# Kernel optimization log

Measured on AMD Instinct MI355X. Metric: run time of the kernel, lower is better.

Reference implementation:

```python
import jax, jax.numpy as jnp
import numpy as np

B, S, D, H = 4, 2048, 1024, 16
DK = D // H

def setup_inputs() -> dict:
    key = jax.random.key(0)
    ks = jax.random.split(key, 11)
    s = 1.0 / np.sqrt(D)
    return {
        "query": jax.random.normal(ks[0], (B, S, D), jnp.float32),
        "key_": jax.random.normal(ks[1], (B, S, D), jnp.float32),
        "value": jax.random.normal(ks[2], (B, S, D), jnp.float32),
        "Wq": jax.random.uniform(ks[3], (D, D), jnp.float32, -s, s),
        "bq": jax.random.uniform(ks[4], (D,), jnp.float32, -s, s),
        "Wk": jax.random.uniform(ks[5], (D, D), jnp.float32, -s, s),
        "bk": jax.random.uniform(ks[6], (D,), jnp.float32, -s, s),
        "Wv": jax.random.uniform(ks[7], (D, D), jnp.float32, -s, s),
        "bv": jax.random.uniform(ks[8], (D,), jnp.float32, -s, s),
        "Wo": jax.random.uniform(ks[9], (D, D), jnp.float32, -s, s),
        "bo": jax.random.uniform(ks[10], (D,), jnp.float32, -s, s),
    }

def _split_heads(x):
    # [B,S,D] -> [B,H,S,DK]
    b, s, _ = x.shape
    return x.reshape(b, s, H, DK).transpose(0, 2, 1, 3)

def reference(query, key_, value, Wq, bq, Wk, bk, Wv, bv, Wo, bo):
    Q = _split_heads(query @ Wq.T + bq)
    K = _split_heads(key_ @ Wk.T + bk)
    V = _split_heads(value @ Wv.T + bv)
    scores = jnp.einsum('bhqd,bhkd->bhqk', Q, K) / np.sqrt(DK).astype(np.float32)
    attn = jax.nn.softmax(scores, axis=-1)
    ctx = jnp.einsum('bhqk,bhkd->bhqd', attn, V)  # [B,H,S,DK]
    ctx = ctx.transpose(0, 2, 1, 3).reshape(query.shape[0], -1, D)
    return ctx @ Wo.T + bo
```

## Files before the change

kernel.cpp:

```cpp
#include <hip/hip_runtime.h>
#include <hip/hip_bf16.h>
#include <math.h>


#define B_SZ   4
#define S_LEN  2048
#define D_DIM  1024
#define NH     16
#define DKD    64
#define M_TOT  (B_SZ * S_LEN)

typedef __bf16 bf16_t;
typedef bf16_t bf16x8 __attribute__((ext_vector_type(8)));
typedef bf16_t bf16x4 __attribute__((ext_vector_type(4)));
typedef float  f32x4  __attribute__((ext_vector_type(4)));

typedef __attribute__((address_space(1))) void gvoid;
typedef __attribute__((address_space(3))) void lvoid;

extern "C" __device__ float __ocml_native_exp2_f32(float);

__global__ __launch_bounds__(256)
void cvt_kernel(const float* __restrict__ src, bf16_t* __restrict__ dst, int n4)
{
    const int i = blockIdx.x * blockDim.x + threadIdx.x;
    if (i < n4) {
        f32x4 v = *(const f32x4*)(src + (size_t)i * 4);
        bf16x4 o;
        #pragma unroll
        for (int j = 0; j < 4; ++j) o[j] = (bf16_t)v[j];
        *(bf16x4*)(dst + (size_t)i * 4) = o;
    }
}

__global__ __launch_bounds__(256, 2)
void qkv_gemm(const float* __restrict__ Aq, const float* __restrict__ Ak,
              const float* __restrict__ Av,
              const bf16_t* __restrict__ Wqb, const bf16_t* __restrict__ Wkb,
              const bf16_t* __restrict__ Wvb,
              const float* __restrict__ bq, const float* __restrict__ bk,
              const float* __restrict__ bv,
              bf16_t* __restrict__ Qw, bf16_t* __restrict__ Kw,
              bf16_t* __restrict__ Vt, float qscale)
{
    constexpr int K = 1024, N = 1024;
    constexpr int BM = 128, BN = 128, BK = 32;

    __shared__ __align__(16) bf16_t lA[BM * BK];
    __shared__ __align__(16) bf16_t lB[BN * BK];

    const int z = blockIdx.z;
    const float* A  = (z == 0) ? Aq : (z == 1) ? Ak : Av;
    const bf16_t* W = (z == 0) ? Wqb : (z == 1) ? Wkb : Wvb;
    const float* bias = (z == 0) ? bq : (z == 1) ? bk : bv;
    const float scale = (z == 0) ? qscale : 1.0f;

    const int tid  = threadIdx.x;
    const int wave = tid >> 6;
    const int lane = tid & 63;

    const int row0 = blockIdx.x * BM;
    const int col0 = blockIdx.y * BN;

    const int wr = (wave >> 1) * 64;
    const int wc = (wave & 1) * 64;

    f32x4 acc[4][4] = {};

    const int frow = lane & 15;
    const int kq   = (lane >> 4) * 8;

    const int r0c = tid >> 2;
    const int k0c = (tid & 3) * 8;
    const int r1c = (256 + tid) >> 2;
    const int k1c = k0c;

    f32x4 pa[2][2];
    {
        const float* g0 = A + (size_t)(row0 + r0c) * K + k0c;
        const float* g1 = A + (size_t)(row0 + r1c) * K + k1c;
        pa[0][0] = *(const f32x4*)g0;  pa[0][1] = *(const f32x4*)(g0 + 4);
        pa[1][0] = *(const f32x4*)g1;  pa[1][1] = *(const f32x4*)(g1 + 4);
    }

    for (int k0 = 0; k0 < K; k0 += BK) {
        __syncthreads();
        #pragma unroll
        for (int p = 0; p < 2; ++p) {
            bf16x8 a8;
            #pragma unroll
            for (int j = 0; j < 4; ++j) {
                a8[j]     = (bf16_t)pa[p][0][j];
                a8[4 + j] = (bf16_t)pa[p][1][j];
            }
            *(bf16x8*)(lA + (p * 256 + tid) * 8) = a8;
        }
        #pragma unroll
        for (int c = 0; c < 2; ++c) {
            const int chunk = c * 4 + wave;
            const int e     = chunk * 512 + lane * 8;
            const int rr    = e >> 5;
            const int kk    = e & 31;
            __builtin_amdgcn_global_load_lds((gvoid*)(W + (size_t)(col0 + rr) * K + k0 + kk),
                                             (lvoid*)(lB + chunk * 512), 16, 0, 0);
        }
        __syncthreads();

        if (k0 + BK < K) {
            const float* g0 = A + (size_t)(row0 + r0c) * K + (k0 + BK) + k0c;
            const float* g1 = A + (size_t)(row0 + r1c) * K + (k0 + BK) + k1c;
            pa[0][0] = *(const f32x4*)g0;  pa[0][1] = *(const f32x4*)(g0 + 4);
            pa[1][0] = *(const f32x4*)g1;  pa[1][1] = *(const f32x4*)(g1 + 4);
        }

        bf16x8 af[4], bfr[4];
        #pragma unroll
        for (int i = 0; i < 4; ++i) {
            af[i]  = *(const bf16x8*)(lA + (wr + i * 16 + frow) * BK + kq);
            bfr[i] = *(const bf16x8*)(lB + (wc + i * 16 + frow) * BK + kq);
        }
        #pragma unroll
        for (int i = 0; i < 4; ++i)
            #pragma unroll
            for (int j = 0; j < 4; ++j)
                acc[i][j] = __builtin_amdgcn_mfma_f32_16x16x32_bf16(af[i], bfr[j], acc[i][j], 0, 0, 0);
    }

    const int rb   = (lane >> 4) * 4;
    const int ccol = lane & 15;
    #pragma unroll
    for (int j = 0; j < 4; ++j) {
        const int n = col0 + wc + j * 16 + ccol;
        const float bvv = bias[n];
        #pragma unroll
        for (int i = 0; i < 4; ++i) {
            const int m = row0 + wr + i * 16 + rb;
            if (z == 2) {
                bf16x4 o4;
                #pragma unroll
                for (int r = 0; r < 4; ++r) o4[r] = (bf16_t)(acc[i][j][r] + bvv);
                *(bf16x4*)(Vt + (size_t)n * M_TOT + m) = o4;
            } else {
                bf16_t* Cp = (z == 0) ? Qw : Kw;
                #pragma unroll
                for (int r = 0; r < 4; ++r)
                    Cp[(size_t)(m + r) * N + n] = (bf16_t)((acc[i][j][r] + bvv) * scale);
            }
        }
    }
}

__global__ __launch_bounds__(256, 2)
void gemm_out(const bf16_t* __restrict__ A, const bf16_t* __restrict__ Bt,
              const float* __restrict__ bias, float* __restrict__ C)
{
    constexpr int K = 1024, N = 1024;
    constexpr int BM = 128, BK = 32;

    __shared__ __align__(16) bf16_t lA[BM * BK];
    __shared__ __align__(16) bf16_t lB[128 * BK];

    const int tid  = threadIdx.x;
    const int wave = tid >> 6;
    const int lane = tid & 63;

    const int row0 = blockIdx.x * BM;
    const int col0 = blockIdx.y * 128;

    const int wr = (wave >> 1) * 64;
    const int wc = (wave & 1) * 64;

    f32x4 acc[4][4] = {};

    const int frow = lane & 15;
    const int kq   = (lane >> 4) * 8;

    for (int k0 = 0; k0 < K; k0 += BK) {
        __syncthreads();
        #pragma unroll
        for (int c = 0; c < 2; ++c) {
            const int chunk = c * 4 + wave;
            const int e     = chunk * 512 + lane * 8;
            const int r     = e >> 5;
            const int kk    = e & 31;
            __builtin_amdgcn_global_load_lds((gvoid*)(A + (size_t)(row0 + r) * K + k0 + kk),
                                             (lvoid*)(lA + chunk * 512), 16, 0, 0);
            __builtin_amdgcn_global_load_lds((gvoid*)(Bt + (size_t)(col0 + r) * K + k0 + kk),
                                             (lvoid*)(lB + chunk * 512), 16, 0, 0);
        }
        __syncthreads();

        bf16x8 af[4], bfr[4];
        #pragma unroll
        for (int i = 0; i < 4; ++i) {
            af[i]  = *(const bf16x8*)(lA + (wr + i * 16 + frow) * BK + kq);
            bfr[i] = *(const bf16x8*)(lB + (wc + i * 16 + frow) * BK + kq);
        }
        #pragma unroll
        for (int i = 0; i < 4; ++i)
            #pragma unroll
            for (int j = 0; j < 4; ++j)
                acc[i][j] = __builtin_amdgcn_mfma_f32_16x16x32_bf16(af[i], bfr[j], acc[i][j], 0, 0, 0);
    }

    const int rb   = (lane >> 4) * 4;
    const int ccol = lane & 15;
    #pragma unroll
    for (int j = 0; j < 4; ++j) {
        const int n = col0 + wc + j * 16 + ccol;
        const float bvv = bias[n];
        #pragma unroll
        for (int i = 0; i < 4; ++i) {
            const int m = row0 + wr + i * 16 + rb;
            #pragma unroll
            for (int r = 0; r < 4; ++r)
                C[(size_t)(m + r) * N + n] = acc[i][j][r] + bvv;
        }
    }
}

__global__ __launch_bounds__(256, 4)
void attn_mfma(const bf16_t* __restrict__ Qg, const bf16_t* __restrict__ Kg,
               const bf16_t* __restrict__ Vt, bf16_t* __restrict__ ctx)
{
    constexpr int PSTR = 72;
    __shared__ __align__(16) bf16_t lK[64 * PSTR];
    __shared__ __align__(16) bf16_t lV[64 * PSTR];
    __shared__ __align__(16) bf16_t lP[4][32 * PSTR];

    const int tid  = threadIdx.x;
    const int wave = tid >> 6;
    const int lane = tid & 63;
    const int qd   = lane >> 4;
    const int c    = lane & 15;

    const int bh   = blockIdx.x >> 4;
    const int qblk = blockIdx.x & 15;
    const int b    = bh >> 4;
    const int h    = bh & 15;

    const int q0 = qblk * 128 + wave * 32;

    const bf16_t* Qb = Qg + ((size_t)(b * S_LEN + q0)) * D_DIM + h * DKD;
    const bf16_t* Kb = Kg + ((size_t)(b * S_LEN)) * D_DIM + h * DKD;
    const bf16_t* Vb = Vt + ((size_t)(h * DKD)) * M_TOT + b * S_LEN;

    bf16_t* Pw = &lP[wave][0];

    bf16x8 qf[2][2];
    #pragma unroll
    for (int qt = 0; qt < 2; ++qt)
        #pragma unroll
        for (int ks = 0; ks < 2; ++ks)
            qf[qt][ks] = *(const bf16x8*)(Qb + (size_t)(qt * 16 + c) * D_DIM + ks * 32 + qd * 8);

    bf16x8 ones;
    #pragma unroll
    for (int i = 0; i < 8; ++i) ones[i] = (bf16_t)1.0f;

    f32x4 oacc[4][2] = {};
    f32x4 lacc[2]    = {};

    for (int kt = 0; kt < S_LEN; kt += 64) {
        __syncthreads();
        #pragma unroll
        for (int cc = 0; cc < 2; ++cc) {
            const int ch  = cc * 256 + tid;
            const int row = ch >> 3;
            const int c8  = ch & 7;
            bf16x8 kv = *(const bf16x8*)(Kb + (size_t)(kt + row) * D_DIM + c8 * 8);
            bf16x8 vv = *(const bf16x8*)(Vb + (size_t)row * M_TOT + kt + c8 * 8);
            *(bf16x8*)(lK + row * PSTR + c8 * 8) = kv;
            *(bf16x8*)(lV + row * PSTR + c8 * 8) = vv;
        }
        __syncthreads();

        bf16x8 kf[4][2];
        #pragma unroll
        for (int i = 0; i < 4; ++i)
            #pragma unroll
            for (int ks = 0; ks < 2; ++ks)
                kf[i][ks] = *(const bf16x8*)(lK + (i * 16 + c) * PSTR + ks * 32 + qd * 8);

        f32x4 st[4][2] = {};
        #pragma unroll
        for (int ks = 0; ks < 2; ++ks)
            #pragma unroll
            for (int i = 0; i < 4; ++i)
                #pragma unroll
                for (int qt = 0; qt < 2; ++qt)
                    st[i][qt] = __builtin_amdgcn_mfma_f32_16x16x32_bf16(kf[i][ks], qf[qt][ks], st[i][qt], 0, 0, 0);

        bf16x8 vf[4][2];
        #pragma unroll
        for (int fm = 0; fm < 4; ++fm)
            #pragma unroll
            for (int ks = 0; ks < 2; ++ks)
                vf[fm][ks] = *(const bf16x8*)(lV + (fm * 16 + c) * PSTR + ks * 32 + qd * 8);

        #pragma unroll
        for (int i = 0; i < 4; ++i)
            #pragma unroll
            for (int qt = 0; qt < 2; ++qt) {
                bf16x4 pw;
                #pragma unroll
                for (int r = 0; r < 4; ++r)
                    pw[r] = (bf16_t)__ocml_native_exp2_f32(st[i][qt][r]);
                *(bf16x4*)(Pw + (qt * 16 + c) * PSTR + i * 16 + qd * 4) = pw;
            }

        #pragma unroll
        for (int qn = 0; qn < 2; ++qn)
            #pragma unroll
            for (int ks = 0; ks < 2; ++ks) {
                bf16x8 pf = *(const bf16x8*)(Pw + (qn * 16 + c) * PSTR + ks * 32 + qd * 8);
                lacc[qn] = __builtin_amdgcn_mfma_f32_16x16x32_bf16(ones, pf, lacc[qn], 0, 0, 0);
                #pragma unroll
                for (int fm = 0; fm < 4; ++fm)
                    oacc[fm][qn] = __builtin_amdgcn_mfma_f32_16x16x32_bf16(vf[fm][ks], pf, oacc[fm][qn], 0, 0, 0);
            }
    }

    #pragma unroll
    for (int qn = 0; qn < 2; ++qn) {
        const float linv = 1.0f / lacc[qn][0];
        bf16_t* op = ctx + ((size_t)(b * S_LEN + q0 + qn * 16 + c)) * D_DIM + h * DKD + qd * 4;
        #pragma unroll
        for (int fm = 0; fm < 4; ++fm) {
            bf16x4 o4;
            #pragma unroll
            for (int r = 0; r < 4; ++r) o4[r] = (bf16_t)(oacc[fm][qn][r] * linv);
            *(bf16x4*)(op + fm * 16) = o4;
        }
    }
}

extern "C" void kernel_launch(void* const* d_in, const int* in_sizes, int n_in,
                              void* d_out, int out_size, void* d_ws, size_t ws_size,
                              hipStream_t stream)
{
    const float* query = (const float*)d_in[0];
    const float* key_  = (const float*)d_in[1];
    const float* value = (const float*)d_in[2];
    const float* Wq    = (const float*)d_in[3];
    const float* bq    = (const float*)d_in[4];
    const float* Wk    = (const float*)d_in[5];
    const float* bk    = (const float*)d_in[6];
    const float* Wv    = (const float*)d_in[7];
    const float* bv    = (const float*)d_in[8];
    const float* Wo    = (const float*)d_in[9];
    const float* bo    = (const float*)d_in[10];
    float* out = (float*)d_out;

    const size_t mat  = (size_t)M_TOT * D_DIM;
    const size_t wmat = (size_t)D_DIM * D_DIM;

    bf16_t* t0 = (bf16_t*)d_ws;
    bf16_t* w0 = t0 + mat;
    bf16_t* Qw = w0 + wmat;
    bf16_t* Kw = Qw + mat;
    bf16_t* Vt = Kw + mat;
    bf16_t* w1 = t0;
    bf16_t* w2 = t0 + wmat;

    const int gcvt_w = (int)(wmat / 4 / 256);
    const float qscale = 0.18033688011112042f;

    cvt_kernel<<<gcvt_w, 256, 0, stream>>>(Wq, w0, (int)(wmat / 4));
    cvt_kernel<<<gcvt_w, 256, 0, stream>>>(Wk, w1, (int)(wmat / 4));
    cvt_kernel<<<gcvt_w, 256, 0, stream>>>(Wv, w2, (int)(wmat / 4));

    qkv_gemm<<<dim3(M_TOT / 128, D_DIM / 128, 3), 256, 0, stream>>>(
        query, key_, value, w0, w1, w2, bq, bk, bv, Qw, Kw, Vt, qscale);

    attn_mfma<<<dim3(B_SZ * NH * (S_LEN / 128)), 256, 0, stream>>>(Qw, Kw, Vt, t0);

    cvt_kernel<<<gcvt_w, 256, 0, stream>>>(Wo, w0, (int)(wmat / 4));
    gemm_out<<<dim3(M_TOT / 128, D_DIM / 128), 256, 0, stream>>>(t0, w0, bo, out);
}
```

Baseline: 356.1 us.

## Batch weight conversions into one launch and reorder grids for cache locality

The four fp32-to-bf16 weight conversions are merged into a single launch that uses blockIdx.z to pick the matrix, and Wo is converted up front into its own workspace slot. Both GEMM grids are transposed so that blocks launched back to back share the same row tile of A and sweep across columns. The attention block index is remapped so consecutive blocks cover 8 heads for the same query block. The goal is fewer launches and better L2 reuse of activation tiles, at the cost of a larger workspace to hold the fourth weight matrix.

```diff
diff --git a/kernel.cpp b/kernel.cpp
--- a/kernel.cpp
+++ b/kernel.cpp
@@ -21,8 +21,14 @@
 extern "C" __device__ float __ocml_native_exp2_f32(float);
 
 __global__ __launch_bounds__(256)
-void cvt_kernel(const float* __restrict__ src, bf16_t* __restrict__ dst, int n4)
-{
+void cvt4_kernel(const float* __restrict__ s0, const float* __restrict__ s1,
+                 const float* __restrict__ s2, const float* __restrict__ s3,
+                 bf16_t* __restrict__ d0, bf16_t* __restrict__ d1,
+                 bf16_t* __restrict__ d2, bf16_t* __restrict__ d3, int n4)
+{
+    const int zz = blockIdx.z;
+    const float* src = (zz == 0) ? s0 : (zz == 1) ? s1 : (zz == 2) ? s2 : s3;
+    bf16_t*      dst = (zz == 0) ? d0 : (zz == 1) ? d1 : (zz == 2) ? d2 : d3;
     const int i = blockIdx.x * blockDim.x + threadIdx.x;
     if (i < n4) {
         f32x4 v = *(const f32x4*)(src + (size_t)i * 4);
@@ -44,10 +50,10 @@
               bf16_t* __restrict__ Vt, float qscale)
 {
     constexpr int K = 1024, N = 1024;
-    constexpr int BM = 128, BN = 128, BK = 32;
+    constexpr int BM = 128, BK = 32;
 
     __shared__ __align__(16) bf16_t lA[BM * BK];
-    __shared__ __align__(16) bf16_t lB[BN * BK];
+    __shared__ __align__(16) bf16_t lB[128 * BK];
 
     const int z = blockIdx.z;
     const float* A  = (z == 0) ? Aq : (z == 1) ? Ak : Av;
@@ -59,8 +65,8 @@
     const int wave = tid >> 6;
     const int lane = tid & 63;
 
-    const int row0 = blockIdx.x * BM;
-    const int col0 = blockIdx.y * BN;
+    const int col0 = blockIdx.x * 128;
+    const int row0 = blockIdx.y * BM;
 
     const int wr = (wave >> 1) * 64;
     const int wc = (wave & 1) * 64;
@@ -73,12 +79,11 @@
     const int r0c = tid >> 2;
     const int k0c = (tid & 3) * 8;
     const int r1c = (256 + tid) >> 2;
-    const int k1c = k0c;
 
     f32x4 pa[2][2];
     {
         const float* g0 = A + (size_t)(row0 + r0c) * K + k0c;
-        const float* g1 = A + (size_t)(row0 + r1c) * K + k1c;
+        const float* g1 = A + (size_t)(row0 + r1c) * K + k0c;
         pa[0][0] = *(const f32x4*)g0;  pa[0][1] = *(const f32x4*)(g0 + 4);
         pa[1][0] = *(const f32x4*)g1;  pa[1][1] = *(const f32x4*)(g1 + 4);
     }
@@ -108,7 +113,7 @@
 
         if (k0 + BK < K) {
             const float* g0 = A + (size_t)(row0 + r0c) * K + (k0 + BK) + k0c;
-            const float* g1 = A + (size_t)(row0 + r1c) * K + (k0 + BK) + k1c;
+            const float* g1 = A + (size_t)(row0 + r1c) * K + (k0 + BK) + k0c;
             pa[0][0] = *(const f32x4*)g0;  pa[0][1] = *(const f32x4*)(g0 + 4);
             pa[1][0] = *(const f32x4*)g1;  pa[1][1] = *(const f32x4*)(g1 + 4);
         }
@@ -164,8 +169,8 @@
     const int wave = tid >> 6;
     const int lane = tid & 63;
 
-    const int row0 = blockIdx.x * BM;
-    const int col0 = blockIdx.y * 128;
+    const int col0 = blockIdx.x * 128;
+    const int row0 = blockIdx.y * BM;
 
     const int wr = (wave >> 1) * 64;
     const int wc = (wave & 1) * 64;
@@ -234,8 +239,9 @@
     const int qd   = lane >> 4;
     const int c    = lane & 15;
 
-    const int bh   = blockIdx.x >> 4;
-    const int qblk = blockIdx.x & 15;
+    const int g    = blockIdx.x;
+    const int bh   = ((g >> 7) << 3) | (g & 7);
+    const int qblk = (g >> 3) & 15;
     const int b    = bh >> 4;
     const int h    = bh & 15;
 
@@ -362,19 +368,18 @@
     bf16_t* Vt = Kw + mat;
     bf16_t* w1 = t0;
     bf16_t* w2 = t0 + wmat;
+    bf16_t* w3 = Vt + mat;
 
     const int gcvt_w = (int)(wmat / 4 / 256);
     const float qscale = 0.18033688011112042f;
 
-    cvt_kernel<<<gcvt_w, 256, 0, stream>>>(Wq, w0, (int)(wmat / 4));
-    cvt_kernel<<<gcvt_w, 256, 0, stream>>>(Wk, w1, (int)(wmat / 4));
-    cvt_kernel<<<gcvt_w, 256, 0, stream>>>(Wv, w2, (int)(wmat / 4));
-
-    qkv_gemm<<<dim3(M_TOT / 128, D_DIM / 128, 3), 256, 0, stream>>>(
+    cvt4_kernel<<<dim3(gcvt_w, 1, 4), 256, 0, stream>>>(
+        Wq, Wk, Wv, Wo, w0, w1, w2, w3, (int)(wmat / 4));
+
+    qkv_gemm<<<dim3(D_DIM / 128, M_TOT / 128, 3), 256, 0, stream>>>(
         query, key_, value, w0, w1, w2, bq, bk, bv, Qw, Kw, Vt, qscale);
 
     attn_mfma<<<dim3(B_SZ * NH * (S_LEN / 128)), 256, 0, stream>>>(Qw, Kw, Vt, t0);
 
-    cvt_kernel<<<gcvt_w, 256, 0, stream>>>(Wo, w0, (int)(wmat / 4));
-    gemm_out<<<dim3(M_TOT / 128, D_DIM / 128), 256, 0, stream>>>(t0, w0, bo, out);
-}
+    gemm_out<<<dim3(D_DIM / 128, M_TOT / 128), 256, 0, stream>>>(t0, w3, bo, out);
+}
```

Measured after the change: 368.2 us. 1.03x slower.
